# Kernel tuning notes

Hardware: AMD Instinct MI355X
Metric: run time of the kernel (lower is better)

Reference implementation:

```python
import jax, jax.numpy as jnp
import numpy as np


def setup_inputs() -> dict:
    key = jax.random.key(0)
    ks = jax.random.split(key, 5)
    bsz, input_size, hidden_size, level_hidden = 8192, 1024, 1024, 64
    d_in = input_size + hidden_size
    return {
        "input": jax.random.normal(ks[0], (bsz, input_size), dtype=jnp.float32),
        "h_prev": jax.random.normal(ks[1], (bsz, hidden_size), dtype=jnp.float32),
        "c_prev": jax.random.normal(ks[2], (bsz, hidden_size), dtype=jnp.float32),
        "W_lstm": jax.random.normal(ks[3], (4 * hidden_size, d_in), dtype=jnp.float32) * (1.0 / np.sqrt(d_in)),
        "W_level": jax.random.normal(ks[4], (2 * level_hidden, d_in), dtype=jnp.float32) * (1.0 / np.sqrt(d_in)),
    }


def reference(input, h_prev, c_prev, W_lstm, W_level):
    hidden_size = h_prev.shape[1]
    level_hidden = W_level.shape[0] // 2
    n_repeat = hidden_size // level_hidden

    combined = jnp.concatenate([input, h_prev], axis=-1)  # (B, in+hid)
    lstm_out = combined @ W_lstm.T                        # (B, 4*hid)
    cc_i, cc_f, cc_o, cc_g = jnp.split(lstm_out, 4, axis=1)
    level_out = combined @ W_level.T                      # (B, 2*lvl)
    cc_i_h, cc_f_h = jnp.split(level_out, 2, axis=1)

    i = jax.nn.sigmoid(cc_i)
    f = jax.nn.sigmoid(cc_f)
    o = jax.nn.sigmoid(cc_o)
    g = jnp.tanh(cc_g)

    p_f = jax.nn.softmax(cc_f_h, axis=-1)
    p_i = jax.nn.softmax(cc_i_h, axis=-1)
    f_h = jnp.cumsum(p_f, axis=-1)                         # forward cumsum
    i_h = jnp.flip(jnp.cumsum(jnp.flip(p_i, -1), axis=-1), -1)  # reverse cumsum

    # expand each level gate value across its chunk of the hidden dim
    i_h = jnp.repeat(i_h, n_repeat, axis=1)                # (B, hid)
    f_h = jnp.repeat(f_h, n_repeat, axis=1)

    w = i_h * f_h
    c = w * (f * c_prev + i * g) + (f_h - w) * c_prev + (i_h - w) * g
    h = o * jnp.tanh(c)
    return (h, c)
```

## Files before the change

kernel.cpp:

```cpp
#include <hip/hip_runtime.h>


typedef unsigned short u16;
typedef __attribute__((ext_vector_type(8))) short bf16x8;
typedef __attribute__((ext_vector_type(8))) short s8v;
typedef __attribute__((ext_vector_type(4))) float f32x4;
typedef __attribute__((ext_vector_type(4))) float v4f;

#define GLDS(g, l) __builtin_amdgcn_global_load_lds(                      \
    (const __attribute__((address_space(1))) void*)(g),                   \
    (__attribute__((address_space(3))) void*)(l), 16, 0, 0)

__device__ __forceinline__ u16 f2bf(float x) {
  unsigned u = __builtin_bit_cast(unsigned, x);
  u += 0x7FFFu + ((u >> 16) & 1u);
  return (u16)(u >> 16);
}
__device__ __forceinline__ float bf2f(u16 h) {
  unsigned u = ((unsigned)h) << 16;
  return __builtin_bit_cast(float, u);
}
__device__ __forceinline__ float fsig(float x) { return 1.0f / (1.0f + __expf(-x)); }
__device__ __forceinline__ float ftanhf(float x) { float e = __expf(2.0f * x); return 1.0f - 2.0f / (e + 1.0f); }

__global__ __launch_bounds__(256) void k_convert(
    const float* __restrict__ inp, const float* __restrict__ hprev,
    const float* __restrict__ wl, const float* __restrict__ wlev,
    u16* __restrict__ Ahi, u16* __restrict__ Alo,
    u16* __restrict__ Whi, u16* __restrict__ Wlo)
{
  const int GA = (8192 * 2048) / 8;
  const int GW = (4224 * 2048) / 8;
  for (int gi = blockIdx.x * 256 + threadIdx.x; gi < GA + GW; gi += gridDim.x * 256) {
    if (gi < GA) {
      int e = gi << 3; int row = e >> 11, col = e & 2047;
      const float* src = (col < 1024) ? (inp + row * 1024 + col)
                                      : (hprev + row * 1024 + (col - 1024));
      v4f a = *(const v4f*)src, b = *(const v4f*)(src + 4);
      float vv[8] = {a.x, a.y, a.z, a.w, b.x, b.y, b.z, b.w};
      s8v hi, lo;
#pragma unroll
      for (int j = 0; j < 8; ++j) {
        u16 h = f2bf(vv[j]);
        hi[j] = (short)h;
        lo[j] = (short)f2bf(vv[j] - bf2f(h));
      }
      *(s8v*)(Ahi + e) = hi;
      *(s8v*)(Alo + e) = lo;
    } else {
      int e = (gi - GA) << 3; int n = e >> 11, k = e & 2047;
      const float* src;
      if (n < 4096) { int j = n >> 2, g = n & 3; src = wl + (size_t)((g << 10) | j) * 2048 + k; }
      else          { src = wlev + (size_t)(n - 4096) * 2048 + k; }
      v4f a = *(const v4f*)src, b = *(const v4f*)(src + 4);
      float vv[8] = {a.x, a.y, a.z, a.w, b.x, b.y, b.z, b.w};
      s8v hi, lo;
#pragma unroll
      for (int j = 0; j < 8; ++j) {
        u16 h = f2bf(vv[j]);
        hi[j] = (short)h;
        lo[j] = (short)f2bf(vv[j] - bf2f(h));
      }
      *(s8v*)(Whi + e) = hi;
      if (n >= 4096) *(s8v*)(Wlo + (size_t)(n - 4096) * 2048 + k) = lo;
    }
  }
}

__global__ __launch_bounds__(256) void k_gemm_level(
    const u16* __restrict__ Ahi, const u16* __restrict__ Alo,
    const u16* __restrict__ Whi, const u16* __restrict__ Wlo,
    float* __restrict__ part)
{
  __shared__ __align__(16) u16 smem[4 * 8192];
  u16 *Ah = smem, *Al = smem + 8192, *Bh = smem + 16384, *Bl = smem + 24576;
  const int tid = threadIdx.x, lane = tid & 63, wid = tid >> 6;
  const int wm = wid >> 1, wn = wid & 1;
  const int rm = blockIdx.x, s = blockIdx.y;
  const int lrow = lane >> 3, lcolE = (lane & 7) << 3;
  const int c16 = lane & 15, r16 = lane >> 4;
  f32x4 acc[4][4] = {};
  const u16* aBaseH = Ahi + (size_t)(rm << 7) * 2048;
  const u16* aBaseL = Alo + (size_t)(rm << 7) * 2048;
  const u16* bBaseH = Whi + (size_t)4096 * 2048;

  for (int kt = 0; kt < 4; ++kt) {
    const int k0 = (s << 8) + (kt << 6);
#pragma unroll
    for (int q = 0; q < 4; ++q) {
      const int ca = (wid << 2) + q;
      size_t roff = (size_t)((ca << 3) + lrow) * 2048 + k0 + lcolE;
      GLDS(aBaseH + roff, Ah + (ca << 9));
      GLDS(aBaseL + roff, Al + (ca << 9));
      GLDS(bBaseH + roff, Bh + (ca << 9));
      GLDS(Wlo + roff,    Bl + (ca << 9));
    }
    __syncthreads();
#pragma unroll
    for (int ks = 0; ks < 2; ++ks) {
      bf16x8 ah[4], al[4];
#pragma unroll
      for (int i = 0; i < 4; ++i) {
        int off = ((wm << 6) + (i << 4) + c16) * 64 + (ks << 5) + (r16 << 3);
        ah[i] = *(const bf16x8*)(Ah + off);
        al[i] = *(const bf16x8*)(Al + off);
      }
#pragma unroll
      for (int j = 0; j < 4; ++j) {
        int off = ((wn << 6) + (j << 4) + c16) * 64 + (ks << 5) + (r16 << 3);
        bf16x8 bh = *(const bf16x8*)(Bh + off);
        bf16x8 bl = *(const bf16x8*)(Bl + off);
#pragma unroll
        for (int i = 0; i < 4; ++i) {
          acc[i][j] = __builtin_amdgcn_mfma_f32_16x16x32_bf16(ah[i], bh, acc[i][j], 0, 0, 0);
          acc[i][j] = __builtin_amdgcn_mfma_f32_16x16x32_bf16(al[i], bh, acc[i][j], 0, 0, 0);
          acc[i][j] = __builtin_amdgcn_mfma_f32_16x16x32_bf16(ah[i], bl, acc[i][j], 0, 0, 0);
        }
      }
    }
    __syncthreads();
  }
#pragma unroll
  for (int mi = 0; mi < 4; ++mi)
#pragma unroll
    for (int ni = 0; ni < 4; ++ni)
#pragma unroll
      for (int r = 0; r < 4; ++r) {
        int ml = (wm << 6) + (mi << 4) + (r16 << 2) + r;
        int nl = (wn << 6) + (ni << 4) + c16;
        part[(size_t)((s << 13) + (rm << 7) + ml) * 128 + nl] = acc[mi][ni][r];
      }
}

__global__ __launch_bounds__(256) void k_softmax(
    const float* __restrict__ part, float* __restrict__ ih, float* __restrict__ fh)
{
  const int tid = threadIdx.x, lane = tid & 63, w = tid >> 6;
  const int row = blockIdx.x * 4 + w;
  float vi = 0.f, vf = 0.f;
#pragma unroll
  for (int s = 0; s < 8; ++s) {
    vi += part[(size_t)((s << 13) + row) * 128 + lane];
    vf += part[(size_t)((s << 13) + row) * 128 + 64 + lane];
  }
  float mi = vi, mf = vf;
#pragma unroll
  for (int d = 1; d < 64; d <<= 1) {
    mi = fmaxf(mi, __shfl_xor(mi, d, 64));
    mf = fmaxf(mf, __shfl_xor(mf, d, 64));
  }
  float ei = __expf(vi - mi), ef = __expf(vf - mf);
  float si = ei, sf = ef;
#pragma unroll
  for (int d = 1; d < 64; d <<= 1) {
    si += __shfl_xor(si, d, 64);
    sf += __shfl_xor(sf, d, 64);
  }
  float pi = ei / si, pf = ef / sf;
  float ci = pi, cf = pf;
#pragma unroll
  for (int d = 1; d < 64; d <<= 1) {
    float t = __shfl_up(ci, d, 64); if (lane >= d) ci += t;
    float u = __shfl_up(cf, d, 64); if (lane >= d) cf += u;
  }
  ih[(row << 6) + lane] = 1.0f - (ci - pi);
  fh[(row << 6) + lane] = cf;
}

__global__ __launch_bounds__(512, 2) void k_gemm_main(
    const u16* __restrict__ Ab, const u16* __restrict__ Wb,
    const float* __restrict__ cprev, const float* __restrict__ ihp,
    const float* __restrict__ fhp, float* __restrict__ out)
{
  __shared__ __align__(16) u16 smem[49152];
  const int tid = threadIdx.x, lane = tid & 63, wid = tid >> 6;
  const int wm = wid >> 2, wn = wid & 3;
  const int c16 = lane & 15, r16 = lane >> 4;

  const int bx = blockIdx.x;
  const int nb = (bx & 7) * 64 + (bx >> 3);
  const int rm = nb >> 4, cm = nb & 15;

  const int sr = tid >> 2;
  const int slq = tid & 3;
  const int sx = (slq ^ (sr & 3)) << 3;
  const u16* pa = Ab + (size_t)(rm * 256 + sr) * 2048 + sx;
  const u16* pb = Wb + (size_t)(cm * 256 + sr) * 2048 + sx;
  char* const ldsT = (char*)smem + (wid << 10);

  const int xa = (r16 ^ (c16 & 3)) << 4;
  const int abase = (wm * 128 + c16) * 64 + xa;
  const int bbase = 16384 + (wn * 64 + c16) * 64 + xa;

  f32x4 acc[8][4] = {};

#define STAGEG(tile, op, buf) do {                                     \
    const u16* s_ = ((op) ? pb : pa) + (size_t)(tile) * 32;            \
    char* d_ = ldsT + (buf) * 32768 + (op) * 16384;                    \
    GLDS(s_, d_);                                                      \
    GLDS(s_ + 128 * 2048, d_ + 8192);                                  \
  } while (0)

#define TILE(buf, t2, buf2, dostage) do {                              \
    bf16x8 aX[8], bS0, bS1, bS2, bS3;                                  \
    _Pragma("unroll")                                                  \
    for (int i = 0; i < 8; ++i)                                        \
      aX[i] = *(const bf16x8*)((const char*)smem + (buf) * 32768 + abase + i * 1024); \
    bS0 = *(const bf16x8*)((const char*)smem + (buf) * 32768 + bbase);         \
    bS1 = *(const bf16x8*)((const char*)smem + (buf) * 32768 + bbase + 1024);  \
    if (dostage) STAGEG((t2), 0, (buf2));                              \
    __builtin_amdgcn_s_barrier();                                      \
    asm volatile("s_waitcnt lgkmcnt(0)" ::: "memory");                 \
    __builtin_amdgcn_s_setprio(1);                                     \
    _Pragma("unroll")                                                  \
    for (int i = 0; i < 8; ++i) {                                      \
      acc[i][0] = __builtin_amdgcn_mfma_f32_16x16x32_bf16(aX[i], bS0, acc[i][0], 0, 0, 0); \
      acc[i][1] = __builtin_amdgcn_mfma_f32_16x16x32_bf16(aX[i], bS1, acc[i][1], 0, 0, 0); \
    }                                                                  \
    __builtin_amdgcn_s_setprio(0);                                     \
    __builtin_amdgcn_s_barrier();                                      \
    bS2 = *(const bf16x8*)((const char*)smem + (buf) * 32768 + bbase + 2048);  \
    bS3 = *(const bf16x8*)((const char*)smem + (buf) * 32768 + bbase + 3072);  \
    if (dostage) STAGEG((t2), 1, (buf2));                              \
    __builtin_amdgcn_s_barrier();                                      \
    asm volatile("s_waitcnt lgkmcnt(0)" ::: "memory");                 \
    __builtin_amdgcn_s_setprio(1);                                     \
    _Pragma("unroll")                                                  \
    for (int i = 0; i < 8; ++i) {                                      \
      acc[i][2] = __builtin_amdgcn_mfma_f32_16x16x32_bf16(aX[i], bS2, acc[i][2], 0, 0, 0); \
      acc[i][3] = __builtin_amdgcn_mfma_f32_16x16x32_bf16(aX[i], bS3, acc[i][3], 0, 0, 0); \
    }                                                                  \
    __builtin_amdgcn_s_setprio(0);                                     \
    if (dostage) asm volatile("s_waitcnt vmcnt(4)" ::: "memory");      \
    __builtin_amdgcn_s_barrier();                                      \
  } while (0)

  STAGEG(0, 0, 0); STAGEG(0, 1, 0);
  STAGEG(1, 0, 1); STAGEG(1, 1, 1);
  asm volatile("s_waitcnt vmcnt(4)" ::: "memory");
  __builtin_amdgcn_s_barrier();

  for (int u = 0; u < 21; ++u) {
    const int t0 = u * 3;
    TILE(0, (t0 + 2) & 63, 2, 1);
    TILE(1, (t0 + 3) & 63, 0, 1);
    TILE(2, (t0 + 4) & 63, 1, 1);
  }
  TILE(0, 0, 0, 0);
#undef TILE
#undef STAGEG

  asm volatile("s_waitcnt vmcnt(0)" ::: "memory");
  __builtin_amdgcn_s_barrier();

  float* epi = (float*)smem;
#define EPIPASS(p) do {                                                \
    if (wm == ((p) >> 1)) {                                            \
      _Pragma("unroll")                                                \
      for (int iq = 0; iq < 4; ++iq)                                   \
        _Pragma("unroll")                                              \
        for (int j = 0; j < 4; ++j)                                    \
          _Pragma("unroll")                                            \
          for (int r = 0; r < 4; ++r) {                                \
            float v = acc[((p) & 1) * 4 + iq][j][r];                   \
            v = ((c16 & 3) == 3) ? ftanhf(v) : fsig(v);                \
            epi[(iq * 16 + r16 * 4 + r) * 256 + wn * 64 + j * 16 + c16] = v; \
          }                                                            \
    }                                                                  \
    __syncthreads();                                                   \
    _Pragma("unroll")                                                  \
    for (int e = 0; e < 8; ++e) {                                      \
      int idx = (e << 9) + tid;                                        \
      int m = idx >> 6, jl = idx & 63;                                 \
      v4f v = *(const v4f*)(epi + m * 256 + (jl << 2));                \
      int rowg = rm * 256 + (p) * 64 + m;                              \
      int jg = cm * 64 + jl;                                           \
      float cp = cprev[rowg * 1024 + jg];                              \
      int lv = jg >> 4;                                                \
      float vih = ihp[(rowg << 6) + lv], vfh = fhp[(rowg << 6) + lv];  \
      float iv = v.x, fv = v.y, ov = v.z, gv = v.w;                    \
      float wq = vih * vfh;                                            \
      float c = wq * (fv * cp + iv * gv) + (vfh - wq) * cp + (vih - wq) * gv; \
      float h = ov * ftanhf(c);                                        \
      out[rowg * 1024 + jg] = h;                                       \
      out[8388608 + rowg * 1024 + jg] = c;                             \
    }                                                                  \
    __syncthreads();                                                   \
  } while (0)
  EPIPASS(0); EPIPASS(1); EPIPASS(2); EPIPASS(3);
#undef EPIPASS
}

extern "C" void kernel_launch(void* const* d_in, const int* in_sizes, int n_in,
                              void* d_out, int out_size, void* d_ws, size_t ws_size,
                              hipStream_t stream) {
  (void)in_sizes; (void)n_in; (void)out_size; (void)ws_size;
  const float* inp   = (const float*)d_in[0];
  const float* hprev = (const float*)d_in[1];
  const float* cprev = (const float*)d_in[2];
  const float* wl    = (const float*)d_in[3];
  const float* wlev  = (const float*)d_in[4];
  float* out = (float*)d_out;
  char* ws = (char*)d_ws;

  u16* Ahi  = (u16*)(ws);
  u16* Alo  = (u16*)(ws + 33554432);
  u16* Whi  = (u16*)(ws + 67108864);
  u16* Wlo  = (u16*)(ws + 84410368);
  float* part = (float*)(ws + 84934656);
  float* ih   = (float*)(ws + 118489088);
  float* fh   = (float*)(ws + 120586240);

  k_convert<<<dim3(2048), dim3(256), 0, stream>>>(inp, hprev, wl, wlev, Ahi, Alo, Whi, Wlo);
  k_gemm_level<<<dim3(64, 8), dim3(256), 0, stream>>>(Ahi, Alo, Whi, Wlo, part);
  k_softmax<<<dim3(2048), dim3(256), 0, stream>>>(part, ih, fh);
  k_gemm_main<<<dim3(512), dim3(512), 0, stream>>>(Ahi, Whi, cprev, ih, fh, out);
}
```

Measured before the change: 244.0 us.

## Double K-tile to 64 with two-buffer LDS ping-pong and quadrant MFMA schedule

The main GEMM loop now stages K=64 per tile (two 32-wide halves) into 128KB of LDS. It uses two buffers instead of three 32-wide buffers and changes the LDS swizzle to match. Each tile is split into four quadrant MFMA phases with interleaved LDS reads, and the next tile's global-to-LDS loads are issued mid-tile into the same buffer. The aim is to halve the number of loop iterations and the barrier/waitcnt overhead per unit of K and to raise reuse per load. In exchange it uses more LDS per block and needs more barriers per tile, and reusing the buffer in flight risks ordering hazards.

```diff
diff --git a/kernel.cpp b/kernel.cpp
--- a/kernel.cpp
+++ b/kernel.cpp
@@ -172,7 +172,7 @@
     const float* __restrict__ cprev, const float* __restrict__ ihp,
     const float* __restrict__ fhp, float* __restrict__ out)
 {
-  __shared__ __align__(16) u16 smem[49152];
+  __shared__ __align__(16) u16 smem[65536];
   const int tid = threadIdx.x, lane = tid & 63, wid = tid >> 6;
   const int wm = wid >> 2, wn = wid & 3;
   const int c16 = lane & 15, r16 = lane >> 4;
@@ -183,75 +183,93 @@
 
   const int sr = tid >> 2;
   const int slq = tid & 3;
-  const int sx = (slq ^ (sr & 3)) << 3;
+  const int sx = (slq ^ ((sr >> 1) & 3)) << 3;
   const u16* pa = Ab + (size_t)(rm * 256 + sr) * 2048 + sx;
   const u16* pb = Wb + (size_t)(cm * 256 + sr) * 2048 + sx;
   char* const ldsT = (char*)smem + (wid << 10);
 
-  const int xa = (r16 ^ (c16 & 3)) << 4;
-  const int abase = (wm * 128 + c16) * 64 + xa;
-  const int bbase = 16384 + (wn * 64 + c16) * 64 + xa;
+  const char* const lbase = (const char*)smem;
+  const int xsl = (r16 ^ ((c16 >> 1) & 3)) << 4;
+  const int aBase = wm * 8192 + c16 * 64 + xsl;
+  const int bBase = 32768 + (wn >> 1) * 8192 + ((wn & 1) * 64 + c16) * 64 + xsl;
 
   f32x4 acc[8][4] = {};
-
-#define STAGEG(tile, op, buf) do {                                     \
-    const u16* s_ = ((op) ? pb : pa) + (size_t)(tile) * 32;            \
-    char* d_ = ldsT + (buf) * 32768 + (op) * 16384;                    \
-    GLDS(s_, d_);                                                      \
-    GLDS(s_ + 128 * 2048, d_ + 8192);                                  \
+  bf16x8 aX[4][2];
+  bf16x8 bS[2][2][2];
+
+#define RD_A(buf_, ih_)                                                \
+    _Pragma("unroll")                                                  \
+    for (int fi = 0; fi < 4; ++fi)                                     \
+      _Pragma("unroll")                                                \
+      for (int kh = 0; kh < 2; ++kh)                                   \
+        aX[fi][kh] = *(const bf16x8*)(lbase + (buf_) * 65536 +         \
+            kh * 16384 + aBase + (ih_) * 4096 + fi * 1024);
+
+#define RD_B(buf_, jh_)                                                \
+    _Pragma("unroll")                                                  \
+    for (int fj = 0; fj < 2; ++fj)                                     \
+      _Pragma("unroll")                                                \
+      for (int kh = 0; kh < 2; ++kh)                                   \
+        bS[jh_][fj][kh] = *(const bf16x8*)(lbase + (buf_) * 65536 +    \
+            kh * 16384 + bBase + (jh_) * 2048 + fj * 1024);
+
+#define MM(ih_, jh_)                                                   \
+    _Pragma("unroll")                                                  \
+    for (int fi = 0; fi < 4; ++fi)                                     \
+      _Pragma("unroll")                                                \
+      for (int fj = 0; fj < 2; ++fj)                                   \
+        _Pragma("unroll")                                              \
+        for (int kh = 0; kh < 2; ++kh)                                 \
+          acc[(ih_) * 4 + fi][(jh_) * 2 + fj] =                        \
+              __builtin_amdgcn_mfma_f32_16x16x32_bf16(aX[fi][kh],      \
+                  bS[jh_][fj][kh], acc[(ih_) * 4 + fi][(jh_) * 2 + fj], 0, 0, 0);
+
+#define STAGE8(t2_, buf_) do {                                         \
+    _Pragma("unroll")                                                  \
+    for (int c = 0; c < 8; ++c) {                                      \
+      const int op_ = c >> 2, kh_ = (c >> 1) & 1, rh_ = c & 1;         \
+      GLDS((op_ ? pb : pa) + rh_ * 262144 + (t2_) * 64 + kh_ * 32,     \
+           ldsT + (buf_) * 65536 + op_ * 32768 + kh_ * 16384 + rh_ * 8192); \
+    }                                                                  \
   } while (0)
 
-#define TILE(buf, t2, buf2, dostage) do {                              \
-    bf16x8 aX[8], bS0, bS1, bS2, bS3;                                  \
-    _Pragma("unroll")                                                  \
-    for (int i = 0; i < 8; ++i)                                        \
-      aX[i] = *(const bf16x8*)((const char*)smem + (buf) * 32768 + abase + i * 1024); \
-    bS0 = *(const bf16x8*)((const char*)smem + (buf) * 32768 + bbase);         \
-    bS1 = *(const bf16x8*)((const char*)smem + (buf) * 32768 + bbase + 1024);  \
-    if (dostage) STAGEG((t2), 0, (buf2));                              \
-    __builtin_amdgcn_s_barrier();                                      \
-    asm volatile("s_waitcnt lgkmcnt(0)" ::: "memory");                 \
-    __builtin_amdgcn_s_setprio(1);                                     \
-    _Pragma("unroll")                                                  \
-    for (int i = 0; i < 8; ++i) {                                      \
-      acc[i][0] = __builtin_amdgcn_mfma_f32_16x16x32_bf16(aX[i], bS0, acc[i][0], 0, 0, 0); \
-      acc[i][1] = __builtin_amdgcn_mfma_f32_16x16x32_bf16(aX[i], bS1, acc[i][1], 0, 0, 0); \
+#define BAR() __builtin_amdgcn_s_barrier()
+#define LGKM0() asm volatile("s_waitcnt lgkmcnt(0)" ::: "memory")
+#define PRIO(v) __builtin_amdgcn_s_setprio(v)
+
+#define TILE(buf_, t2_, dostage_, lastvm_) do {                        \
+    RD_A(buf_, 0); RD_B(buf_, 0);                                      \
+    BAR(); LGKM0(); PRIO(1); MM(0, 0); PRIO(0); BAR();                 \
+    RD_B(buf_, 1);                                                     \
+    BAR(); LGKM0(); PRIO(1); MM(0, 1); PRIO(0); BAR();                 \
+    RD_A(buf_, 1);                                                     \
+    BAR(); LGKM0(); PRIO(1); MM(1, 0); PRIO(0); BAR();                 \
+    if (dostage_) {                                                    \
+      STAGE8((t2_), (buf_));                                           \
+      asm volatile("s_waitcnt vmcnt(8)" ::: "memory");                 \
     }                                                                  \
-    __builtin_amdgcn_s_setprio(0);                                     \
-    __builtin_amdgcn_s_barrier();                                      \
-    bS2 = *(const bf16x8*)((const char*)smem + (buf) * 32768 + bbase + 2048);  \
-    bS3 = *(const bf16x8*)((const char*)smem + (buf) * 32768 + bbase + 3072);  \
-    if (dostage) STAGEG((t2), 1, (buf2));                              \
-    __builtin_amdgcn_s_barrier();                                      \
-    asm volatile("s_waitcnt lgkmcnt(0)" ::: "memory");                 \
-    __builtin_amdgcn_s_setprio(1);                                     \
-    _Pragma("unroll")                                                  \
-    for (int i = 0; i < 8; ++i) {                                      \
-      acc[i][2] = __builtin_amdgcn_mfma_f32_16x16x32_bf16(aX[i], bS2, acc[i][2], 0, 0, 0); \
-      acc[i][3] = __builtin_amdgcn_mfma_f32_16x16x32_bf16(aX[i], bS3, acc[i][3], 0, 0, 0); \
-    }                                                                  \
-    __builtin_amdgcn_s_setprio(0);                                     \
-    if (dostage) asm volatile("s_waitcnt vmcnt(4)" ::: "memory");      \
-    __builtin_amdgcn_s_barrier();                                      \
+    if (lastvm_) asm volatile("s_waitcnt vmcnt(0)" ::: "memory");      \
+    BAR(); PRIO(1); MM(1, 1); PRIO(0); BAR();                          \
   } while (0)
 
-  STAGEG(0, 0, 0); STAGEG(0, 1, 0);
-  STAGEG(1, 0, 1); STAGEG(1, 1, 1);
-  asm volatile("s_waitcnt vmcnt(4)" ::: "memory");
-  __builtin_amdgcn_s_barrier();
-
-  for (int u = 0; u < 21; ++u) {
-    const int t0 = u * 3;
-    TILE(0, (t0 + 2) & 63, 2, 1);
-    TILE(1, (t0 + 3) & 63, 0, 1);
-    TILE(2, (t0 + 4) & 63, 1, 1);
-  }
-  TILE(0, 0, 0, 0);
+  STAGE8(0, 0);
+  STAGE8(1, 1);
+  asm volatile("s_waitcnt vmcnt(8)" ::: "memory");
+  BAR();
+
+  for (int u = 0; u < 15; ++u) {
+    TILE(0, 2 * u + 2, 1, 0);
+    TILE(1, 2 * u + 3, 1, 0);
+  }
+  TILE(0, 0, 0, 1);
+  TILE(1, 0, 0, 0);
 #undef TILE
-#undef STAGEG
-
-  asm volatile("s_waitcnt vmcnt(0)" ::: "memory");
-  __builtin_amdgcn_s_barrier();
+#undef STAGE8
+#undef MM
+#undef RD_B
+#undef RD_A
+
+  BAR();
 
   float* epi = (float*)smem;
 #define EPIPASS(p) do {                                                \
```

Result: slower. 254.9 us (+4.5%).
